# Kernel tuning notes

Hardware: AMD Instinct MI355X
Metric: run time of the kernel (lower is better)

## Reference

```python
import jax, jax.numpy as jnp
import numpy as np

EPS_LN = 1e-5

def _layernorm(v, w, b):
    m = jnp.mean(v, axis=-1, keepdims=True)
    var = jnp.mean((v - m) ** 2, axis=-1, keepdims=True)
    return (v - m) / jnp.sqrt(var + EPS_LN) * w + b

def _safe_norm(d):
    # norm over last axis, keepdims, with exact 0 on the diagonal and finite grads
    sq = jnp.sum(d * d, axis=-1, keepdims=True)
    safe = jnp.where(sq > 0, sq, 1.0)
    return jnp.sqrt(safe) * (sq > 0), sq

def _lin(v, w, b):
    return v @ w.T + b

def setup_inputs() -> dict:
    key = jax.random.key(0)
    B, N, F = 4, 256, 128
    ks = jax.random.split(key, 24)
    def w(k, o, i):
        return jax.random.normal(k, (o, i), dtype=jnp.float32) / np.sqrt(i)
    def bvec(k, o):
        return jax.random.normal(k, (o,), dtype=jnp.float32) * 0.01
    inp = {
        "x": jax.random.normal(ks[0], (B, N, 3), dtype=jnp.float32),
        "h": jax.random.normal(ks[1], (B, N, F), dtype=jnp.float32),
        "x0": jax.random.normal(ks[2], (B, N, 3), dtype=jnp.float32),
        "lnh_w": jnp.ones((F,), jnp.float32), "lnh_b": jnp.zeros((F,), jnp.float32),
        "lnx_w": jnp.ones((3,), jnp.float32), "lnx_b": jnp.zeros((3,), jnp.float32),
        "edg1_w": w(ks[3], F, 2 * F + 2), "edg1_b": bvec(ks[4], F),
        "edg2_w": w(ks[5], F, F), "edg2_b": bvec(ks[6], F),
        "edgi_w": w(ks[7], 1, F), "edgi_b": bvec(ks[8], 1),
        "node1_w": w(ks[9], F, 2 * F), "node1_b": bvec(ks[10], F),
        "node2_w": w(ks[11], F, F), "node2_b": bvec(ks[12], F),
        "cor1_w": w(ks[13], F, 2 * F + 2), "cor1_b": bvec(ks[14], F),
        "cor2_w": w(ks[15], F, F), "cor2_b": bvec(ks[16], F),
        "cor3_w": w(ks[17], 1, F), "cor3_b": bvec(ks[18], 1),
    }
    return inp

def reference(x, h, x0, lnh_w, lnh_b, lnx_w, lnx_b,
              edg1_w, edg1_b, edg2_w, edg2_b, edgi_w, edgi_b,
              node1_w, node1_b, node2_w, node2_b,
              cor1_w, cor1_b, cor2_w, cor2_b, cor3_w, cor3_b):
    B, N, F = h.shape
    silu = jax.nn.silu
    # pairwise distances (computed BEFORE layernorm, as in the original)
    d0 = x0[:, :, None, :] - x0[:, None, :, :]          # (B,N,N,3)
    r0, _ = _safe_norm(d0)                               # (B,N,N,1)
    diff = x[:, :, None, :] - x[:, None, :, :]           # (B,N,N,3)
    r, dsq = _safe_norm(diff)                            # (B,N,N,1) each
    h_ln = _layernorm(h, lnh_w, lnh_b)                   # (B,N,F)
    x_ln = _layernorm(x, lnx_w, lnx_b)                   # (B,N,3)
    # h_cart[b,i,j] = concat(h_ln[b,i], h_ln[b,j], |x_i-x_j|^2, |x0_i-x0_j|)
    hi = jnp.broadcast_to(h_ln[:, :, None, :], (B, N, N, F))
    hj = jnp.broadcast_to(h_ln[:, None, :, :], (B, N, N, F))
    pair = jnp.concatenate([hi, hj, dsq, r0], axis=-1)   # (B,N,N,2F+2)
    # edge MLP
    m = silu(_lin(pair, edg1_w, edg1_b))
    m = silu(_lin(m, edg2_w, edg2_b))                    # (B,N,N,F)
    e = jax.nn.sigmoid(_lin(m, edgi_w, edgi_b))          # (B,N,N,1)
    e = e * (1.0 - jnp.eye(N, dtype=e.dtype)[None, :, :, None])
    # node update: sum over second node index j (dim=-2)
    agg = jnp.sum(e * m, axis=2)                         # (B,N,F)
    nu = silu(_lin(jnp.concatenate([h_ln, agg], axis=-1), node1_w, node1_b))
    h_next = h_ln + _lin(nu, node2_w, node2_b)
    # coordinate update
    cw = silu(_lin(pair, cor1_w, cor1_b))
    cw = silu(_lin(cw, cor2_w, cor2_b))
    cw = _lin(cw, cor3_w, cor3_b)                        # (B,N,N,1)
    cor_shift = diff / (r + 1.0)                         # (B,N,N,3)
    x_next = x_ln + jnp.sum(cw * cor_shift, axis=2)      # (B,N,3)
    return (x_next, h_next)
```

## Files before the change

kernel.cpp:

```cpp
#include <hip/hip_runtime.h>

typedef unsigned int UI;
typedef unsigned short u16;

typedef short short8 __attribute__((ext_vector_type(8)));
typedef float floatx4 __attribute__((ext_vector_type(4)));
typedef unsigned short ushort8 __attribute__((ext_vector_type(8)));

__device__ __forceinline__ float bf2f(u16 u) {
  return __uint_as_float(((UI)u) << 16);
}
__device__ __forceinline__ u16 f2bf(float x) {
  UI u = __float_as_uint(x);
  u += 0x7fffu + ((u >> 16) & 1u);
  return (u16)(u >> 16);
}
__device__ __forceinline__ float fsigmoid(float v) {
  float e = __builtin_amdgcn_exp2f(-1.44269504089f * v);
  return __builtin_amdgcn_rcpf(1.0f + e);
}
__device__ __forceinline__ float fsilu(float v) { return v * fsigmoid(v); }

__global__ __launch_bounds__(256) void k1_ln(
    const float* __restrict__ h, const float* __restrict__ x,
    const float* __restrict__ lnh_w, const float* __restrict__ lnh_b,
    const float* __restrict__ lnx_w, const float* __restrict__ lnx_b,
    const float* __restrict__ edg1_w, const float* __restrict__ cor1_w,
    const float* __restrict__ node1_w, const float* __restrict__ node2_w,
    float* __restrict__ hln, float* __restrict__ xln,
    float* __restrict__ e1T, float* __restrict__ c1T,
    float* __restrict__ n1T, float* __restrict__ n2T) {
  __shared__ float tile[32][33];
  const int bx = blockIdx.x, tid = threadIdx.x;
  if (bx < 128) {
    const int wv = tid >> 6, lane = tid & 63;
#pragma unroll 1
    for (int s = 0; s < 2; ++s) {
      const int n = bx * 8 + wv * 2 + s;
      const float* hp = h + n * 128;
      float v0 = hp[lane], v1 = hp[lane + 64];
      float sum = v0 + v1;
#pragma unroll
      for (int m = 1; m < 64; m <<= 1) sum += __shfl_xor(sum, m);
      float mean = sum * 0.0078125f;
      float d0 = v0 - mean, d1 = v1 - mean;
      float vs = d0 * d0 + d1 * d1;
#pragma unroll
      for (int m = 1; m < 64; m <<= 1) vs += __shfl_xor(vs, m);
      float rstd = __builtin_amdgcn_rcpf(__builtin_amdgcn_sqrtf(vs * 0.0078125f + 1e-5f));
      hln[n * 128 + lane]      = d0 * rstd * lnh_w[lane] + lnh_b[lane];
      hln[n * 128 + lane + 64] = d1 * rstd * lnh_w[lane + 64] + lnh_b[lane + 64];
      if (lane == 0) {
        float a = x[n * 3], b2 = x[n * 3 + 1], c = x[n * 3 + 2];
        float m3 = (a + b2 + c) * (1.f / 3.f);
        float va = (a - m3) * (a - m3) + (b2 - m3) * (b2 - m3) + (c - m3) * (c - m3);
        float rs = __builtin_amdgcn_rcpf(__builtin_amdgcn_sqrtf(va * (1.f / 3.f) + 1e-5f));
        xln[n * 3 + 0] = (a - m3) * rs * lnx_w[0] + lnx_b[0];
        xln[n * 3 + 1] = (b2 - m3) * rs * lnx_w[1] + lnx_b[1];
        xln[n * 3 + 2] = (c - m3) * rs * lnx_w[2] + lnx_b[2];
      }
    }
    return;
  }
  int tb = bx - 128;
  const float* src; float* dst; int ld, ntc;
  if (tb < 32)      { src = edg1_w;  dst = e1T; ld = 258; ntc = 8; }
  else if (tb < 64) { src = cor1_w;  dst = c1T; ld = 258; ntc = 8; tb -= 32; }
  else if (tb < 96) { src = node1_w; dst = n1T; ld = 256; ntc = 8; tb -= 64; }
  else              { src = node2_w; dst = n2T; ld = 128; ntc = 4; tb -= 96; }
  const int r0 = (tb / ntc) * 32, c0 = (tb % ntc) * 32;
  const int tx = tid & 31, ty = tid >> 5;
#pragma unroll
  for (int p = 0; p < 4; ++p)
    tile[ty + p * 8][tx] = src[(r0 + ty + p * 8) * ld + c0 + tx];
  __syncthreads();
#pragma unroll
  for (int p = 0; p < 4; ++p)
    dst[(c0 + ty + p * 8) * 128 + r0 + tx] = tile[tx][ty + p * 8];
}

__global__ __launch_bounds__(256, 2) void k2_pre(
    const float* __restrict__ hln,
    const float* __restrict__ e1T, const float* __restrict__ edg1_b,
    const float* __restrict__ c1T, const float* __restrict__ cor1_b,
    const float* __restrict__ edg1_w, const float* __restrict__ cor1_w,
    const float* __restrict__ edg2_w, const float* __restrict__ cor2_w,
    u16* __restrict__ peA, u16* __restrict__ peB,
    u16* __restrict__ pcA, u16* __restrict__ pcB,
    u16* __restrict__ w2e, u16* __restrict__ w2c,
    float* __restrict__ wdwr) {
  const int tid = threadIdx.x;
  const int bx = blockIdx.x;
  if (bx >= 256) {
    const float* src = (bx == 256) ? edg2_w : cor2_w;
    u16* dst = (bx == 256) ? w2e : w2c;
    for (int idx = tid; idx < 16384; idx += 256) {
      int f = idx >> 7, k = idx & 127;
      dst[f * 136 + k] = f2bf(src[idx]);
    }
    const float* w1 = (bx == 256) ? edg1_w : cor1_w;
    float* wvv = wdwr + ((bx == 256) ? 0 : 256);
    if (tid < 128) wvv[tid] = w1[tid * 258 + 256];
    else           wvv[tid] = w1[(tid - 128) * 258 + 257];
    return;
  }
  __shared__ __align__(16) float hl[16][132];
  const int arr = bx >> 6;
  const int nb = bx & 63;
  const int n0 = nb * 16;
  for (int idx = tid; idx < 2048; idx += 256) {
    int r = idx >> 7, k = idx & 127;
    hl[r][k] = hln[(n0 + r) * 128 + k];
  }
  __syncthreads();
  const int f = tid & 127, nh = tid >> 7;
  const float* w1T = (arr < 2) ? e1T : c1T;
  const int off = (arr & 1) ? 128 : 0;
  u16* dst = (arr == 0) ? peA : (arr == 1) ? peB : (arr == 2) ? pcA : pcB;
  float bias = 0.f;
  if (arr == 0) bias = edg1_b[f];
  if (arr == 2) bias = cor1_b[f];
  float wreg[128];
#pragma unroll
  for (int t = 0; t < 128; ++t) wreg[t] = w1T[(off + t) * 128 + f];
#pragma unroll 1
  for (int s = 0; s < 8; ++s) {
    int nl = nh * 8 + s;
    float acc = bias;
#pragma unroll
    for (int t = 0; t < 64; ++t) {
      float2 iv = *(const float2*)&hl[nl][t * 2];
      acc += wreg[2 * t] * iv.x + wreg[2 * t + 1] * iv.y;
    }
    dst[(n0 + nl) * 128 + f] = f2bf(acc);
  }
}

__global__ __launch_bounds__(256, 2) void k3_pair(
    const float* __restrict__ x, const float* __restrict__ x0,
    const u16* __restrict__ peA, const u16* __restrict__ peB,
    const u16* __restrict__ pcA, const u16* __restrict__ pcB,
    const u16* __restrict__ w2e, const u16* __restrict__ w2c,
    const float* __restrict__ wdwr,
    const float* __restrict__ b2e, const float* __restrict__ b2c,
    const float* __restrict__ edgi_w, const float* __restrict__ edgi_b,
    const float* __restrict__ cor3_w, const float* __restrict__ cor3_b,
    float* __restrict__ cw_t, float* __restrict__ partial) {
  __shared__ __align__(16) u16 sW[128 * 136];
  __shared__ __align__(16) u16 sA[16 * 136];
  __shared__ __align__(16) u16 sB[32 * 136];
  __shared__ __align__(16) float swd[128];
  __shared__ __align__(16) float swr[128];
  __shared__ float sxi[16][4], sxj[32][4], sx0i[16][4], sx0j[32][4];
  __shared__ __align__(16) float sagg[16][128];

  const int tid = threadIdx.x;
  const int bx = blockIdx.x;
  const int path = bx >> 9;
  const int rem = bx & 511;
  const int b = rem >> 7;
  const int ib = (rem >> 3) & 15;
  const int jc = rem & 7;
  const int i0 = ib * 16, j0 = jc * 32;

  const u16* pA = path ? pcA : peA;
  const u16* pB = path ? pcB : peB;
  const u16* w2 = path ? w2c : w2e;
  const float* wdp = wdwr + path * 256;
  const float* b2 = path ? b2c : b2e;
  const float* w3 = path ? cor3_w : edgi_w;
  const float w3b = path ? cor3_b[0] : edgi_b[0];

  float* pslot = partial + ((b * 16 + ib) * 8 + jc) * 2048;

  {
    const uint4* src = (const uint4*)w2;
    uint4* dst = (uint4*)sW;
    for (int d = tid; d < 2176; d += 256) dst[d] = src[d];
    const UI* sa_src = (const UI*)(pA + (b * 256 + i0) * 128);
    UI* sa_dst = (UI*)sA;
    for (int d = tid; d < 1024; d += 256) {
      int r = d >> 6, c = d & 63;
      sa_dst[r * 68 + c] = sa_src[d];
    }
    const UI* sb_src = (const UI*)(pB + (b * 256 + j0) * 128);
    UI* sb_dst = (UI*)sB;
    for (int d = tid; d < 2048; d += 256) {
      int r = d >> 6, c = d & 63;
      sb_dst[r * 68 + c] = sb_src[d];
    }
    if (tid < 128) swd[tid] = wdp[tid];
    else           swr[tid - 128] = wdp[tid];
    if (tid < 64) {
      int r = tid >> 2, d = tid & 3;
      sxi[r][d]  = (d < 3) ? x[(b * 256 + i0 + r) * 3 + d] : 0.f;
      sx0i[r][d] = (d < 3) ? x0[(b * 256 + i0 + r) * 3 + d] : 0.f;
    }
    if (tid < 128) {
      int r = tid >> 2, d = tid & 3;
      sxj[r][d]  = (d < 3) ? x[(b * 256 + j0 + r) * 3 + d] : 0.f;
      sx0j[r][d] = (d < 3) ? x0[(b * 256 + j0 + r) * 3 + d] : 0.f;
    }
    float* ag = (float*)sagg;
    for (int d = tid; d < 2048; d += 256) ag[d] = 0.f;
  }
  __syncthreads();

  const int lane = tid & 63;
  const int w = tid >> 6;
  const int il = lane & 15;
  const int ch = lane >> 4;

  float wv[8], bv[8];
#pragma unroll
  for (int nt = 0; nt < 8; ++nt) {
    wv[nt] = w3[nt * 16 + il];
    bv[nt] = b2[nt * 16 + il];
  }

  float aggv[8][4];
#pragma unroll
  for (int nt = 0; nt < 8; ++nt)
#pragma unroll
    for (int q = 0; q < 4; ++q) aggv[nt][q] = 0.f;

#pragma unroll 1
  for (int g = 0; g < 8; ++g) {
    const int jl = w * 8 + g;
    float d0 = sxi[il][0] - sxj[jl][0];
    float d1 = sxi[il][1] - sxj[jl][1];
    float d2 = sxi[il][2] - sxj[jl][2];
    const float dsq = d0 * d0 + d1 * d1 + d2 * d2;
    float e0 = sx0i[il][0] - sx0j[jl][0];
    float e1 = sx0i[il][1] - sx0j[jl][1];
    float e2 = sx0i[il][2] - sx0j[jl][2];
    float q2 = e0 * e0 + e1 * e1 + e2 * e2;
    const float r0v = (q2 > 0.f) ? __builtin_amdgcn_sqrtf(q2) : 0.f;

    floatx4 acc[8];
#pragma unroll
    for (int nt = 0; nt < 8; ++nt)
#pragma unroll
      for (int q = 0; q < 4; ++q) acc[nt][q] = 0.f;

#pragma unroll 1
    for (int ks = 0; ks < 4; ++ks) {
      const int f0 = ks * 32 + ch * 8;
      union { float4 v[2]; float a[8]; } wd8, wr8;
      wd8.v[0] = *(const float4*)&swd[f0];
      wd8.v[1] = *(const float4*)&swd[f0 + 4];
      wr8.v[0] = *(const float4*)&swr[f0];
      wr8.v[1] = *(const float4*)&swr[f0 + 4];
      ushort8 a8 = *(const ushort8*)&sA[il * 136 + f0];
      ushort8 b8 = *(const ushort8*)&sB[jl * 136 + f0];
      short8 af;
#pragma unroll
      for (int e = 0; e < 8; ++e) {
        float xv = bf2f((u16)a8[e]) + bf2f((u16)b8[e]) +
                   dsq * wd8.a[e] + r0v * wr8.a[e];
        af[e] = (short)f2bf(fsilu(xv));
      }
#pragma unroll
      for (int nt = 0; nt < 8; ++nt) {
        short8 bfr = *(const short8*)&sW[(nt * 16 + il) * 136 + f0];
        acc[nt] = __builtin_amdgcn_mfma_f32_16x16x32_bf16(af, bfr, acc[nt], 0, 0, 0);
      }
    }
    float p[4] = {0.f, 0.f, 0.f, 0.f};
#pragma unroll
    for (int nt = 0; nt < 8; ++nt) {
#pragma unroll
      for (int q = 0; q < 4; ++q) {
        float s = fsilu(acc[nt][q] + bv[nt]);
        acc[nt][q] = s;
        p[q] += s * wv[nt];
      }
    }
#pragma unroll
    for (int m = 1; m < 16; m <<= 1) {
#pragma unroll
      for (int q = 0; q < 4; ++q) p[q] += __shfl_xor(p[q], m);
    }
    const int jg = j0 + jl;
    if (path == 0) {
#pragma unroll
      for (int q = 0; q < 4; ++q) {
        int ig = i0 + ch * 4 + q;
        float ev = (ig == jg) ? 0.f : fsigmoid(p[q] + w3b);
#pragma unroll
        for (int nt = 0; nt < 8; ++nt) aggv[nt][q] += ev * acc[nt][q];
      }
    } else {
      if (il == 0) {
        float4 v;
        v.x = p[0] + w3b; v.y = p[1] + w3b; v.z = p[2] + w3b; v.w = p[3] + w3b;
        *(float4*)&cw_t[(b * 256 + jg) * 256 + i0 + ch * 4] = v;
      }
    }
  }
  if (path == 0) {
#pragma unroll
    for (int nt = 0; nt < 8; ++nt)
#pragma unroll
      for (int q = 0; q < 4; ++q)
        atomicAdd(&sagg[ch * 4 + q][nt * 16 + il], aggv[nt][q]);
    __syncthreads();
    const float* ag = (const float*)sagg;
    for (int d = tid; d < 2048; d += 256) pslot[d] = ag[d];
  }
}

__global__ __launch_bounds__(256, 2) void k4_node(
    const float* __restrict__ hln, const float* __restrict__ partial,
    const float* __restrict__ n1T, const float* __restrict__ n1b,
    const float* __restrict__ n2T, const float* __restrict__ n2b,
    float* __restrict__ out) {
  __shared__ __align__(16) float sin_[4][260];
  __shared__ __align__(16) float snu[4][132];
  const int tid = threadIdx.x;
  const int n0 = blockIdx.x * 4;
  for (int idx = tid; idx < 512; idx += 256) {
    int s = idx >> 7, k = idx & 127;
    sin_[s][k] = hln[(n0 + s) * 128 + k];
  }
  for (int idx = tid; idx < 512; idx += 256) {
    int s = idx >> 7, f = idx & 127;
    int n = n0 + s, b = n >> 8, i = n & 255;
    const float* pp = partial + ((b * 16 + (i >> 4)) * 8) * 2048 + (i & 15) * 128 + f;
    float a = 0.f;
#pragma unroll
    for (int j = 0; j < 8; ++j) a += pp[j * 2048];
    sin_[s][128 + f] = a;
  }
  __syncthreads();
  const int f = tid & 127, sh = tid >> 7;
  UI w1r[128];
#pragma unroll
  for (int t = 0; t < 128; ++t) {
    float wa = n1T[(t * 2) * 128 + f];
    float wb = n1T[(t * 2 + 1) * 128 + f];
    w1r[t] = (UI)f2bf(wa) | ((UI)f2bf(wb) << 16);
  }
#pragma unroll 1
  for (int t2 = 0; t2 < 2; ++t2) {
    int s = sh * 2 + t2;
    float acc = n1b[f];
#pragma unroll
    for (int t = 0; t < 128; ++t) {
      UI wp = w1r[t];
      float2 iv = *(const float2*)&sin_[s][t * 2];
      acc += iv.x * bf2f((u16)(wp & 0xffffu)) + iv.y * bf2f((u16)(wp >> 16));
    }
    snu[s][f] = fsilu(acc);
  }
  __syncthreads();
  UI w2r[64];
#pragma unroll
  for (int t = 0; t < 64; ++t) {
    float wa = n2T[(t * 2) * 128 + f];
    float wb = n2T[(t * 2 + 1) * 128 + f];
    w2r[t] = (UI)f2bf(wa) | ((UI)f2bf(wb) << 16);
  }
#pragma unroll 1
  for (int t2 = 0; t2 < 2; ++t2) {
    int s = sh * 2 + t2;
    float acc = n2b[f];
#pragma unroll
    for (int t = 0; t < 64; ++t) {
      UI wp = w2r[t];
      float2 iv = *(const float2*)&snu[s][t * 2];
      acc += iv.x * bf2f((u16)(wp & 0xffffu)) + iv.y * bf2f((u16)(wp >> 16));
    }
    out[3072 + (n0 + s) * 128 + f] = sin_[s][f] + acc;
  }
}

__global__ __launch_bounds__(256) void k5_x(
    const float* __restrict__ x, const float* __restrict__ xln,
    const float* __restrict__ cw_t, float* __restrict__ out) {
  const int wv = threadIdx.x >> 6, lane = threadIdx.x & 63;
  const int n = blockIdx.x * 4 + wv;
  const int b = n >> 8, i = n & 255;
  const float xi0 = x[n * 3 + 0], xi1 = x[n * 3 + 1], xi2 = x[n * 3 + 2];
  float s0 = 0.f, s1 = 0.f, s2 = 0.f;
#pragma unroll
  for (int t = 0; t < 4; ++t) {
    int j = t * 64 + lane;
    const float* xj = x + (b * 256 + j) * 3;
    float d0 = xi0 - xj[0], d1 = xi1 - xj[1], d2 = xi2 - xj[2];
    float q = d0 * d0 + d1 * d1 + d2 * d2;
    float r = (q > 0.f) ? __builtin_amdgcn_sqrtf(q) : 0.f;
    float cw = cw_t[(b * 256 + j) * 256 + i];
    float sc = cw * __builtin_amdgcn_rcpf(r + 1.f);
    s0 += sc * d0; s1 += sc * d1; s2 += sc * d2;
  }
#pragma unroll
  for (int m = 1; m < 64; m <<= 1) {
    s0 += __shfl_xor(s0, m);
    s1 += __shfl_xor(s1, m);
    s2 += __shfl_xor(s2, m);
  }
  if (lane == 0) {
    out[n * 3 + 0] = xln[n * 3 + 0] + s0;
    out[n * 3 + 1] = xln[n * 3 + 1] + s1;
    out[n * 3 + 2] = xln[n * 3 + 2] + s2;
  }
}

extern "C" void kernel_launch(void* const* d_in, const int* in_sizes, int n_in,
                              void* d_out, int out_size, void* d_ws, size_t ws_size,
                              hipStream_t stream) {
  (void)in_sizes; (void)n_in; (void)out_size; (void)ws_size;
  const float* x      = (const float*)d_in[0];
  const float* h      = (const float*)d_in[1];
  const float* x0     = (const float*)d_in[2];
  const float* lnh_w  = (const float*)d_in[3];
  const float* lnh_b  = (const float*)d_in[4];
  const float* lnx_w  = (const float*)d_in[5];
  const float* lnx_b  = (const float*)d_in[6];
  const float* edg1_w = (const float*)d_in[7];
  const float* edg1_b = (const float*)d_in[8];
  const float* edg2_w = (const float*)d_in[9];
  const float* edg2_b = (const float*)d_in[10];
  const float* edgi_w = (const float*)d_in[11];
  const float* edgi_b = (const float*)d_in[12];
  const float* node1_w= (const float*)d_in[13];
  const float* node1_b= (const float*)d_in[14];
  const float* node2_w= (const float*)d_in[15];
  const float* node2_b= (const float*)d_in[16];
  const float* cor1_w = (const float*)d_in[17];
  const float* cor1_b = (const float*)d_in[18];
  const float* cor2_w = (const float*)d_in[19];
  const float* cor2_b = (const float*)d_in[20];
  const float* cor3_w = (const float*)d_in[21];
  const float* cor3_b = (const float*)d_in[22];

  char* ws = (char*)d_ws;
  float* hln  = (float*)(ws);
  float* xln  = (float*)(ws + 524288);
  u16* peA    = (u16*)(ws + 536576);
  u16* peB    = (u16*)(ws + 798720);
  u16* pcA    = (u16*)(ws + 1060864);
  u16* pcB    = (u16*)(ws + 1323008);
  u16* w2e    = (u16*)(ws + 1585152);
  u16* w2c    = (u16*)(ws + 1619968);
  float* wdwr = (float*)(ws + 1654784);
  float* cw_t = (float*)(ws + 1656832);
  float* partial = (float*)(ws + 2705408);
  float* e1T  = (float*)(ws + 6899712);
  float* c1T  = (float*)(ws + 7030784);
  float* n1T  = (float*)(ws + 7161856);
  float* n2T  = (float*)(ws + 7292928);
  float* out  = (float*)d_out;

  hipLaunchKernelGGL(k1_ln, dim3(240), dim3(256), 0, stream,
                     h, x, lnh_w, lnh_b, lnx_w, lnx_b,
                     edg1_w, cor1_w, node1_w, node2_w,
                     hln, xln, e1T, c1T, n1T, n2T);
  hipLaunchKernelGGL(k2_pre, dim3(258), dim3(256), 0, stream,
                     hln, e1T, edg1_b, c1T, cor1_b, edg1_w, cor1_w,
                     edg2_w, cor2_w, peA, peB, pcA, pcB, w2e, w2c, wdwr);
  hipLaunchKernelGGL(k3_pair, dim3(1024), dim3(256), 0, stream,
                     x, x0, peA, peB, pcA, pcB, w2e, w2c, wdwr,
                     edg2_b, cor2_b, edgi_w, edgi_b, cor3_w, cor3_b, cw_t, partial);
  hipLaunchKernelGGL(k4_node, dim3(256), dim3(256), 0, stream,
                     hln, partial, n1T, node1_b, n2T, node2_b, out);
  hipLaunchKernelGGL(k5_x, dim3(256), dim3(256), 0, stream,
                     x, xln, cw_t, out);
}
```

Before: 257.1 us.

## Pre-swizzle weight and A tiles into MFMA fragment order, use packed bf16 convert

```diff
diff --git a/kernel.cpp b/kernel.cpp
--- a/kernel.cpp
+++ b/kernel.cpp
@@ -96,7 +96,8 @@
     u16* dst = (bx == 256) ? w2e : w2c;
     for (int idx = tid; idx < 16384; idx += 256) {
       int f = idx >> 7, k = idx & 127;
-      dst[f * 136 + k] = f2bf(src[idx]);
+      int nt = f >> 4, il = f & 15, ks = k >> 5, ch = (k >> 3) & 3, e = k & 7;
+      dst[(nt * 256 + ks * 64 + ch * 16 + il) * 8 + e] = f2bf(src[idx]);
     }
     const float* w1 = (bx == 256) ? edg1_w : cor1_w;
     float* wvv = wdwr + ((bx == 256) ? 0 : 256);
@@ -146,8 +147,8 @@
     const float* __restrict__ edgi_w, const float* __restrict__ edgi_b,
     const float* __restrict__ cor3_w, const float* __restrict__ cor3_b,
     float* __restrict__ cw_t, float* __restrict__ partial) {
-  __shared__ __align__(16) u16 sW[128 * 136];
-  __shared__ __align__(16) u16 sA[16 * 136];
+  __shared__ __align__(16) u16 sW[2048 * 8];
+  __shared__ __align__(16) u16 sA[256 * 8];
   __shared__ __align__(16) u16 sB[32 * 136];
   __shared__ __align__(16) float swd[128];
   __shared__ __align__(16) float swr[128];
@@ -176,12 +177,11 @@
   {
     const uint4* src = (const uint4*)w2;
     uint4* dst = (uint4*)sW;
-    for (int d = tid; d < 2176; d += 256) dst[d] = src[d];
-    const UI* sa_src = (const UI*)(pA + (b * 256 + i0) * 128);
-    UI* sa_dst = (UI*)sA;
-    for (int d = tid; d < 1024; d += 256) {
-      int r = d >> 6, c = d & 63;
-      sa_dst[r * 68 + c] = sa_src[d];
+    for (int d = tid; d < 2048; d += 256) dst[d] = src[d];
+    {
+      const uint4* sa_src = (const uint4*)(pA + (b * 256 + i0) * 128);
+      int il = tid & 15, ch = (tid >> 4) & 3, ks = tid >> 6;
+      ((uint4*)sA)[tid] = sa_src[il * 16 + ks * 4 + ch];
     }
     const UI* sb_src = (const UI*)(pB + (b * 256 + j0) * 128);
     UI* sb_dst = (UI*)sB;
@@ -251,19 +251,21 @@
       wd8.v[1] = *(const float4*)&swd[f0 + 4];
       wr8.v[0] = *(const float4*)&swr[f0];
       wr8.v[1] = *(const float4*)&swr[f0 + 4];
-      ushort8 a8 = *(const ushort8*)&sA[il * 136 + f0];
+      ushort8 a8 = *(const ushort8*)&sA[(ks * 64 + lane) * 8];
       ushort8 b8 = *(const ushort8*)&sB[jl * 136 + f0];
-      short8 af;
-#pragma unroll
-      for (int e = 0; e < 8; ++e) {
-        float xv = bf2f((u16)a8[e]) + bf2f((u16)b8[e]) +
-                   dsq * wd8.a[e] + r0v * wr8.a[e];
-        af[e] = (short)f2bf(fsilu(xv));
+      union { UI w[4]; short8 s; } afu;
+#pragma unroll
+      for (int e2 = 0; e2 < 4; ++e2) {
+        float s0 = fsilu(bf2f((u16)a8[2 * e2]) + bf2f((u16)b8[2 * e2]) +
+                         dsq * wd8.a[2 * e2] + r0v * wr8.a[2 * e2]);
+        float s1 = fsilu(bf2f((u16)a8[2 * e2 + 1]) + bf2f((u16)b8[2 * e2 + 1]) +
+                         dsq * wd8.a[2 * e2 + 1] + r0v * wr8.a[2 * e2 + 1]);
+        asm("v_cvt_pk_bf16_f32 %0, %1, %2" : "=v"(afu.w[e2]) : "v"(s0), "v"(s1));
       }
 #pragma unroll
       for (int nt = 0; nt < 8; ++nt) {
-        short8 bfr = *(const short8*)&sW[(nt * 16 + il) * 136 + f0];
-        acc[nt] = __builtin_amdgcn_mfma_f32_16x16x32_bf16(af, bfr, acc[nt], 0, 0, 0);
+        short8 bfr = *(const short8*)&sW[(nt * 256 + ks * 64 + lane) * 8];
+        acc[nt] = __builtin_amdgcn_mfma_f32_16x16x32_bf16(afu.s, bfr, acc[nt], 0, 0, 0);
       }
     }
     float p[4] = {0.f, 0.f, 0.f, 0.f};
```

Result: no change. 257.1 us (+0.0%).
